# Kernel optimization log

Hardware: AMD Instinct MI355X
Metric: run time of the kernel (lower is better)

Reference implementation:

```python
import jax, jax.numpy as jnp
import numpy as np

B, N, D, H = 4, 1024, 1024, 16
DH = D // H  # 64
FF = 4 * D   # 4096


def _layernorm(x, w, b, eps=1e-5):
    mu = jnp.mean(x, axis=-1, keepdims=True)
    var = jnp.var(x, axis=-1, keepdims=True)
    return (x - mu) * jax.lax.rsqrt(var + eps) * w + b


def setup_inputs() -> dict:
    key = jax.random.key(0)
    ks = jax.random.split(key, 8)
    s = 0.02
    return {
        "x": jax.random.normal(ks[0], (B, N, D), jnp.float32),
        "ln1_w": jnp.ones((D,), jnp.float32),
        "ln1_b": jnp.zeros((D,), jnp.float32),
        "qkv_w": jax.random.normal(ks[1], (3 * D, D), jnp.float32) * s,
        "qkv_b": jnp.zeros((3 * D,), jnp.float32),
        "proj_l_w": jax.random.normal(ks[2], (H, H), jnp.float32) * s,
        "proj_l_b": jnp.zeros((H,), jnp.float32),
        "proj_w_w": jax.random.normal(ks[3], (H, H), jnp.float32) * s,
        "proj_w_b": jnp.zeros((H,), jnp.float32),
        "out_w": jax.random.normal(ks[4], (D, D), jnp.float32) * s,
        "out_b": jnp.zeros((D,), jnp.float32),
        "gamma1": jnp.ones((D,), jnp.float32),
        "ln2_w": jnp.ones((D,), jnp.float32),
        "ln2_b": jnp.zeros((D,), jnp.float32),
        "fc1_w": jax.random.normal(ks[5], (FF, D), jnp.float32) * s,
        "fc1_b": jnp.zeros((FF,), jnp.float32),
        "fc2_w": jax.random.normal(ks[6], (D, FF), jnp.float32) * s,
        "fc2_b": jnp.zeros((D,), jnp.float32),
        "gamma2": jnp.ones((D,), jnp.float32),
    }


def reference(x, ln1_w, ln1_b, qkv_w, qkv_b, proj_l_w, proj_l_b, proj_w_w,
              proj_w_b, out_w, out_b, gamma1, ln2_w, ln2_b, fc1_w, fc1_b,
              fc2_w, fc2_b, gamma2):
    # ---- LayerScale(TalkingHeadAttention) branch ----
    h = _layernorm(x, ln1_w, ln1_b)
    qkv = h @ qkv_w.T + qkv_b                      # [B,N,3D]
    q, k, v = jnp.split(qkv, 3, axis=-1)
    # [B,N,D] -> [B,H,N,DH]
    reshape = lambda t: t.reshape(B, N, H, DH).transpose(0, 2, 1, 3)
    q, k, v = reshape(q), reshape(k), reshape(v)
    attn = jnp.einsum("bhid,bhjd->bhij", q, k) * (DH ** -0.5)
    # talking-heads mixing before softmax (Linear over head dim)
    attn = jnp.einsum("bhij,gh->bgij", attn, proj_l_w) + proj_l_b[None, :, None, None]
    attn = jax.nn.softmax(attn, axis=-1)
    # talking-heads mixing after softmax
    attn = jnp.einsum("bhij,gh->bgij", attn, proj_w_w) + proj_w_b[None, :, None, None]
    o = jnp.einsum("bhij,bhjd->bhid", attn, v)     # [B,H,N,DH]
    o = o.transpose(0, 2, 1, 3).reshape(B, N, D)
    o = o @ out_w.T + out_b
    x = x + gamma1 * o
    # ---- LayerScale(MLP) branch ----
    h = _layernorm(x, ln2_w, ln2_b)
    h = jax.nn.gelu(h @ fc1_w.T + fc1_b)
    h = h @ fc2_w.T + fc2_b
    return x + gamma2 * h
```

## Files before the change

### kernel.cpp

```cpp
#include <hip/hip_runtime.h>


typedef _Float16 f16x8 __attribute__((ext_vector_type(8)));
typedef _Float16 f16x4 __attribute__((ext_vector_type(4)));
typedef _Float16 f16x2 __attribute__((ext_vector_type(2)));
typedef float f32x4 __attribute__((ext_vector_type(4)));

#define B_ 4
#define N_ 1024
#define D_ 1024
#define H_ 16
#define DH_ 64
#define FF_ 4096
#define M_ (B_ * N_)

__device__ __forceinline__ float gelu_act(float x) {
  float z = 0.7978845608028654f * (x + 0.044715f * x * x * x);
  return x / (1.0f + __expf(-2.0f * z));
}

__device__ __forceinline__ void ld_lds16(const _Float16* g, _Float16* l) {
  __builtin_amdgcn_global_load_lds((const __attribute__((address_space(1))) void*)g,
                                   (__attribute__((address_space(3))) void*)l, 16, 0, 0);
}

__device__ __forceinline__ int swz8(int i) {
  return (((i >> 2) << 1) ^ (i & 3)) & 7;
}
__device__ __forceinline__ int lds_off(int p, int i, int j) {
  int ch = ((j >> 3) ^ swz8(i) ^ ((p >> 2) << 1)) & 7;
  return p * 1032 + i * 64 + (ch << 3) + (j & 7);
}

__global__ __launch_bounds__(256) void cast_f32_f16(const float* __restrict__ in,
                                                    _Float16* __restrict__ out, int n) {
  int i = (blockIdx.x * 256 + threadIdx.x) * 4;
  if (i >= n) return;
  float4 v = *(const float4*)(in + i);
  f16x4 o;
  o[0] = (_Float16)v.x; o[1] = (_Float16)v.y; o[2] = (_Float16)v.z; o[3] = (_Float16)v.w;
  *(f16x4*)(out + i) = o;
}

__global__ __launch_bounds__(256) void prep_w(const float* __restrict__ W1,
                                              const float* __restrict__ W2,
                                              _Float16* __restrict__ w1f,
                                              _Float16* __restrict__ w2f) {
  int t = threadIdx.x;
  w1f[t] = (_Float16)W1[t];
  w2f[t] = (_Float16)W2[t];
}

__global__ __launch_bounds__(256) void vsum_k(const _Float16* __restrict__ vt,
                                              const float* __restrict__ b2,
                                              float* __restrict__ bsum) {
  int g = blockIdx.x, b = blockIdx.y;
  int t = threadIdx.x;
  int d = t >> 2, seg = t & 3;
  const _Float16* row = vt + (size_t)((b * H_ + g) * DH_ + d) * N_ + seg * 256;
  float s = 0.f;
  #pragma unroll
  for (int k = 0; k < 32; k++) {
    f16x8 v = *(const f16x8*)(row + k * 8);
    #pragma unroll
    for (int e = 0; e < 8; e++) s += (float)v[e];
  }
  s += __shfl_xor(s, 1);
  s += __shfl_xor(s, 2);
  if (seg == 0) bsum[b * D_ + g * 64 + d] = b2[g] * s;
}

__global__ __launch_bounds__(256) void ln_f16(const float* __restrict__ x,
                                              const float* __restrict__ w,
                                              const float* __restrict__ b,
                                              _Float16* __restrict__ out) {
  int row = blockIdx.x;
  int tid = threadIdx.x;
  const float* xr = x + (size_t)row * D_;
  float4 v = *(const float4*)(xr + tid * 4);
  float s = v.x + v.y + v.z + v.w;
  float sq = v.x * v.x + v.y * v.y + v.z * v.z + v.w * v.w;
  #pragma unroll
  for (int off = 32; off > 0; off >>= 1) {
    s += __shfl_down(s, off);
    sq += __shfl_down(sq, off);
  }
  __shared__ float red[8];
  int wave = tid >> 6, lane = tid & 63;
  if (lane == 0) { red[wave] = s; red[4 + wave] = sq; }
  __syncthreads();
  float ts = red[0] + red[1] + red[2] + red[3];
  float tq = red[4] + red[5] + red[6] + red[7];
  float mean = ts * (1.0f / (float)D_);
  float var = tq * (1.0f / (float)D_) - mean * mean;
  float rs = rsqrtf(var + 1e-5f);
  float4 wv = *(const float4*)(w + tid * 4);
  float4 bv = *(const float4*)(b + tid * 4);
  f16x4 o;
  o[0] = (_Float16)((v.x - mean) * rs * wv.x + bv.x);
  o[1] = (_Float16)((v.y - mean) * rs * wv.y + bv.y);
  o[2] = (_Float16)((v.z - mean) * rs * wv.z + bv.z);
  o[3] = (_Float16)((v.w - mean) * rs * wv.w + bv.w);
  *(f16x4*)(out + (size_t)row * D_ + tid * 4) = o;
}

template <int EPI, int BN>
__global__ __launch_bounds__(256, 3) void gemm_nt(
    const _Float16* __restrict__ A, const _Float16* __restrict__ W,
    const float* __restrict__ bias, int M, int N, int K,
    _Float16* __restrict__ outB, float* __restrict__ outF,
    const float* __restrict__ res, const float* __restrict__ gamma) {
  __shared__ _Float16 As[128 * 64];
  __shared__ _Float16 Bs[BN * 64];
  int tid = threadIdx.x;
  int wave = tid >> 6, lane = tid & 63;
  int quad = lane >> 4, l16 = lane & 15;
  int wm = wave >> 1, wn = wave & 1;
  int m0 = blockIdx.y * 128, n0 = blockIdx.x * BN;
  int lrow = lane >> 3, lcol = (lane & 7) * 8;
  const int NI = (BN == 128) ? 4 : 2;
  const int WN = (BN == 128) ? 64 : 32;

  f32x4 zero = {0.f, 0.f, 0.f, 0.f};
  f32x4 acc[4][NI];
  #pragma unroll
  for (int i = 0; i < 4; i++)
    #pragma unroll
    for (int j = 0; j < NI; j++) acc[i][j] = zero;

  for (int k0 = 0; k0 < K; k0 += 64) {
    __syncthreads();
    #pragma unroll
    for (int c = 0; c < 4; c++) {
      int rb = c * 32 + wave * 8;
      ld_lds16(A + (size_t)(m0 + rb + lrow) * K + k0 + lcol, As + rb * 64);
      if (BN == 128 || c < 2)
        ld_lds16(W + (size_t)(n0 + rb + lrow) * K + k0 + lcol, Bs + rb * 64);
    }
    __syncthreads();
    #pragma unroll
    for (int ks = 0; ks < 2; ks++) {
      int kk = ks * 32 + quad * 8;
      f16x8 a[4], bfr[NI];
      #pragma unroll
      for (int i = 0; i < 4; i++) a[i] = *(const f16x8*)(As + (wm * 64 + i * 16 + l16) * 64 + kk);
      #pragma unroll
      for (int i = 0; i < NI; i++) bfr[i] = *(const f16x8*)(Bs + (wn * WN + i * 16 + l16) * 64 + kk);
      #pragma unroll
      for (int mi = 0; mi < 4; mi++)
        #pragma unroll
        for (int ni = 0; ni < NI; ni++)
          acc[mi][ni] = __builtin_amdgcn_mfma_f32_16x16x32_f16(a[mi], bfr[ni], acc[mi][ni], 0, 0, 0);
    }
  }

  #pragma unroll
  for (int mi = 0; mi < 4; mi++) {
    int grow_base = m0 + wm * 64 + mi * 16 + quad * 4;
    #pragma unroll
    for (int ni = 0; ni < NI; ni++) {
      int gcol = n0 + wn * WN + ni * 16 + l16;
      float bb = bias[gcol];
      float gm = (EPI == 1) ? gamma[gcol] : 0.f;
      #pragma unroll
      for (int r = 0; r < 4; r++) {
        size_t oi = (size_t)(grow_base + r) * N + gcol;
        float c = acc[mi][ni][r] + bb;
        if (EPI == 0) {
          outB[oi] = (_Float16)c;
        } else if (EPI == 1) {
          outF[oi] = res[oi] + gm * c;
        } else {
          outB[oi] = (_Float16)gelu_act(c);
        }
      }
    }
  }
}

__global__ __launch_bounds__(256) void transpose_v(const _Float16* __restrict__ qkv,
                                                   _Float16* __restrict__ vt) {
  int jt = blockIdx.x;
  int h = blockIdx.y;
  int b = blockIdx.z;
  __shared__ _Float16 tl[64][68];
  int tid = threadIdx.x;
  int j0 = jt * 64;
  #pragma unroll
  for (int k = 0; k < 16; k++) {
    int idx = k * 256 + tid;
    int jr = idx >> 6, dc = idx & 63;
    tl[jr][dc] = qkv[(size_t)(b * N_ + j0 + jr) * (3 * D_) + 2 * D_ + h * 64 + dc];
  }
  __syncthreads();
  #pragma unroll
  for (int k = 0; k < 16; k++) {
    int idx = k * 256 + tid;
    int dr = idx >> 6, jc = idx & 63;
    vt[(size_t)((b * H_ + h) * DH_ + dr) * N_ + j0 + jc] = tl[jc][dr];
  }
}

__global__ __launch_bounds__(1024, 4) void attn_th(
    const _Float16* __restrict__ qkv, const _Float16* __restrict__ vt,
    const _Float16* __restrict__ w1f, const _Float16* __restrict__ w2f,
    const float* __restrict__ b1f, const float* __restrict__ bsum,
    _Float16* __restrict__ ob) {
  __shared__ __align__(16) _Float16 SP[2 * 16512];
  __shared__ float lsum[272];
  _Float16* Sp = SP;
  _Float16* Pp = SP + 16512;

  const int tid = threadIdx.x;
  const int wave = tid >> 6;
  const int lane = tid & 63;
  const int quad = lane >> 4, l16 = lane & 15;
  const int i0 = blockIdx.x * 16;
  const int b = blockIdx.y;
  const size_t bN = (size_t)b * N_;
  const f32x4 zero = {0.f, 0.f, 0.f, 0.f};

  f16x8 qf[2];
  #pragma unroll
  for (int ks = 0; ks < 2; ks++) {
    f16x8 q = *(const f16x8*)(qkv + (bN + i0 + l16) * 3072 + wave * 64 + ks * 32 + quad * 8);
    #pragma unroll
    for (int e = 0; e < 8; e++) q[e] = q[e] * (_Float16)0.125f;
    qf[ks] = q;
  }
  f16x4 w1a = *(const f16x4*)(w1f + l16 * 16 + quad * 4);
  float b1v = b1f[l16];
  f32x4 b1i = {b1v, b1v, b1v, b1v};

  f32x4 uacc[4];
  #pragma unroll
  for (int nt = 0; nt < 4; nt++) uacc[nt] = zero;
  float lacc = 0.f;

  for (int t = 0; t < 16; t++) {
    int j0 = t * 64;
    #pragma unroll
    for (int jb = 0; jb < 4; jb++) {
      const _Float16* kb = qkv + (bN + j0 + jb * 16 + l16) * 3072 + 1024 + wave * 64 + quad * 8;
      f32x4 s = __builtin_amdgcn_mfma_f32_16x16x32_f16(*(const f16x8*)kb, qf[0], zero, 0, 0, 0);
      s = __builtin_amdgcn_mfma_f32_16x16x32_f16(*(const f16x8*)(kb + 32), qf[1], s, 0, 0, 0);
      f16x4 sv;
      #pragma unroll
      for (int r = 0; r < 4; r++) sv[r] = (_Float16)s[r];
      *(f16x4*)(Sp + lds_off(wave, l16, jb * 16 + quad * 4)) = sv;
    }
    __syncthreads();
    #pragma unroll
    for (int cg = 0; cg < 4; cg++) {
      f16x4 sf;
      #pragma unroll
      for (int t4 = 0; t4 < 4; t4++)
        sf[t4] = Sp[lds_off(quad * 4 + t4, wave, cg * 16 + l16)];
      f32x4 a = __builtin_amdgcn_mfma_f32_16x16x16f16(sf, w1a, b1i, 0, 0, 0);
      f16x4 pv;
      #pragma unroll
      for (int r = 0; r < 4; r++) {
        float e = __expf(a[r]);
        lacc += e;
        pv[r] = (_Float16)e;
      }
      *(f16x4*)(Pp + lds_off(l16, wave, cg * 16 + quad * 4)) = pv;
    }
    __syncthreads();
    #pragma unroll
    for (int s = 0; s < 2; s++) {
      f16x8 pf = *(const f16x8*)(Pp + lds_off(wave, l16, s * 32 + quad * 8));
      #pragma unroll
      for (int nt = 0; nt < 4; nt++) {
        f16x8 vf = *(const f16x8*)(vt + (size_t)((b * H_ + wave) * DH_ + nt * 16 + l16) * N_ + j0 + s * 32 + quad * 8);
        uacc[nt] = __builtin_amdgcn_mfma_f32_16x16x32_f16(vf, pf, uacc[nt], 0, 0, 0);
      }
    }
  }

  lacc += __shfl_xor(lacc, 16);
  lacc += __shfl_xor(lacc, 32);
  __syncthreads();
  if (quad == 0) lsum[l16 * 17 + wave] = lacc;
  __syncthreads();
  float invl = 1.0f / lsum[wave * 17 + l16];

  _Float16* Uf = Sp;
  #pragma unroll
  for (int nt = 0; nt < 4; nt++) {
    f16x4 u;
    #pragma unroll
    for (int r = 0; r < 4; r++) u[r] = (_Float16)(uacc[nt][r] * invl);
    *(f16x4*)(Uf + wave * 1092 + l16 * 68 + nt * 16 + quad * 4) = u;
  }
  __syncthreads();

  f16x4 w2a = *(const f16x4*)(w2f + l16 * 16 + quad * 4);
  #pragma unroll
  for (int cg = 0; cg < 4; cg++) {
    f16x4 af;
    #pragma unroll
    for (int t4 = 0; t4 < 4; t4++)
      af[t4] = Uf[(quad * 4 + t4) * 1092 + wave * 68 + cg * 16 + l16];
    f32x4 o = __builtin_amdgcn_mfma_f32_16x16x16f16(af, w2a, zero, 0, 0, 0);
    f32x4 bs = *(const f32x4*)(bsum + b * D_ + l16 * 64 + cg * 16 + quad * 4);
    f16x4 ov;
    #pragma unroll
    for (int r = 0; r < 4; r++) ov[r] = (_Float16)(o[r] + bs[r]);
    *(f16x4*)(ob + (bN + i0 + wave) * D_ + l16 * 64 + cg * 16 + quad * 4) = ov;
  }
}

extern "C" void kernel_launch(void* const* d_in, const int* in_sizes, int n_in,
                              void* d_out, int out_size, void* d_ws, size_t ws_size,
                              hipStream_t stream) {
  const float* x      = (const float*)d_in[0];
  const float* ln1_w  = (const float*)d_in[1];
  const float* ln1_b  = (const float*)d_in[2];
  const float* qkv_w  = (const float*)d_in[3];
  const float* qkv_b  = (const float*)d_in[4];
  const float* plw    = (const float*)d_in[5];
  const float* plb    = (const float*)d_in[6];
  const float* pww    = (const float*)d_in[7];
  const float* pwb    = (const float*)d_in[8];
  const float* out_w  = (const float*)d_in[9];
  const float* out_b  = (const float*)d_in[10];
  const float* gamma1 = (const float*)d_in[11];
  const float* ln2_w  = (const float*)d_in[12];
  const float* ln2_b  = (const float*)d_in[13];
  const float* fc1_w  = (const float*)d_in[14];
  const float* fc1_b  = (const float*)d_in[15];
  const float* fc2_w  = (const float*)d_in[16];
  const float* fc2_b  = (const float*)d_in[17];
  const float* gamma2 = (const float*)d_in[18];
  float* out = (float*)d_out;

  char* ws = (char*)d_ws;
  _Float16* wq   = (_Float16*)(ws + 0);
  _Float16* wo   = (_Float16*)(ws + 6291456);
  _Float16* wf1  = (_Float16*)(ws + 8388608);
  _Float16* wf2  = (_Float16*)(ws + 16777216);
  float*    x1   = (float*)   (ws + 25165824);
  _Float16* ob   = (_Float16*)(ws + 41943040);
  _Float16* hb   = (_Float16*)(ws + 50331648);
  _Float16* qkvb = (_Float16*)(ws + 58720256);
  _Float16* vtb  = (_Float16*)(ws + 83886080);
  _Float16* fb   = (_Float16*)(ws + 58720256);
  _Float16* w1f  = (_Float16*)(ws + 8388608);
  _Float16* w2f  = (_Float16*)(ws + 8388608 + 512);
  float*    bsum = (float*)   (ws + 8388608 + 1024);
  if (ws_size < 92274688) return;

  cast_f32_f16<<<3072 * 1024 / 1024, 256, 0, stream>>>(qkv_w, wq, 3072 * 1024);
  cast_f32_f16<<<1024 * 1024 / 1024, 256, 0, stream>>>(out_w, wo, 1024 * 1024);
  prep_w<<<1, 256, 0, stream>>>(plw, pww, w1f, w2f);

  ln_f16<<<4096, 256, 0, stream>>>(x, ln1_w, ln1_b, hb);
  gemm_nt<0, 128><<<dim3(24, 32), 256, 0, stream>>>(hb, wq, qkv_b, M_, 3 * D_, D_, qkvb, nullptr, nullptr, nullptr);
  transpose_v<<<dim3(16, 16, 4), 256, 0, stream>>>(qkvb, vtb);
  vsum_k<<<dim3(16, 4), 256, 0, stream>>>(vtb, pwb, bsum);
  attn_th<<<dim3(64, 4), 1024, 0, stream>>>(qkvb, vtb, w1f, w2f, plb, bsum, ob);
  gemm_nt<1, 64><<<dim3(16, 32), 256, 0, stream>>>(ob, wo, out_b, M_, D_, D_, nullptr, x1, x, gamma1);

  cast_f32_f16<<<4096 * 1024 / 1024, 256, 0, stream>>>(fc1_w, wf1, 4096 * 1024);
  cast_f32_f16<<<4096 * 1024 / 1024, 256, 0, stream>>>(fc2_w, wf2, 4096 * 1024);

  ln_f16<<<4096, 256, 0, stream>>>(x1, ln2_w, ln2_b, hb);
  gemm_nt<2, 128><<<dim3(32, 32), 256, 0, stream>>>(hb, wf1, fc1_b, M_, FF_, D_, fb, nullptr, nullptr, nullptr);
  gemm_nt<1, 64><<<dim3(16, 32), 256, 0, stream>>>(fb, wf2, fc2_b, M_, D_, FF_, nullptr, out, x1, gamma2);
}
```

Measured before the change: 493.3 us.

## Prefetch K and V tiles into registers in attention loop; tune GEMM occupancy

The attention kernel now loads the next K tile into registers while the current tile is processed, and issues the V fragment loads before the barrier so their latency overlaps the softmax stage. The goal is to hide global memory latency in the QK and PV phases. Separately, the BN=64 GEMMs get a launch-bounds occupancy hint of 4 instead of 3. The extra live registers in the attention kernel could raise register pressure and lower occupancy, and the tighter occupancy bound on the GEMMs could force spills.

```diff
diff --git a/kernel.cpp b/kernel.cpp
--- a/kernel.cpp
+++ b/kernel.cpp
@@ -104,8 +104,8 @@
   *(f16x4*)(out + (size_t)row * D_ + tid * 4) = o;
 }
 
-template <int EPI, int BN>
-__global__ __launch_bounds__(256, 3) void gemm_nt(
+template <int EPI, int BN, int OCC>
+__global__ __launch_bounds__(256, OCC) void gemm_nt(
     const _Float16* __restrict__ A, const _Float16* __restrict__ W,
     const float* __restrict__ bias, int M, int N, int K,
     _Float16* __restrict__ outB, float* __restrict__ outF,
@@ -232,23 +232,45 @@
   float b1v = b1f[l16];
   f32x4 b1i = {b1v, b1v, b1v, b1v};
 
+  const _Float16* vbase = vt + (size_t)((b * H_ + wave) * DH_ + l16) * N_ + quad * 8;
+
   f32x4 uacc[4];
   #pragma unroll
   for (int nt = 0; nt < 4; nt++) uacc[nt] = zero;
   float lacc = 0.f;
 
+  f16x8 kcur[4][2];
+  auto loadK = [&](int j0) {
+    #pragma unroll
+    for (int jb = 0; jb < 4; jb++) {
+      const _Float16* kb = qkv + (bN + j0 + jb * 16 + l16) * 3072 + 1024 + wave * 64 + quad * 8;
+      kcur[jb][0] = *(const f16x8*)kb;
+      kcur[jb][1] = *(const f16x8*)(kb + 32);
+    }
+  };
+  loadK(0);
+
+  f16x8 vreg[4];
+
   for (int t = 0; t < 16; t++) {
     int j0 = t * 64;
+    f32x4 sres[4];
     #pragma unroll
     for (int jb = 0; jb < 4; jb++) {
-      const _Float16* kb = qkv + (bN + j0 + jb * 16 + l16) * 3072 + 1024 + wave * 64 + quad * 8;
-      f32x4 s = __builtin_amdgcn_mfma_f32_16x16x32_f16(*(const f16x8*)kb, qf[0], zero, 0, 0, 0);
-      s = __builtin_amdgcn_mfma_f32_16x16x32_f16(*(const f16x8*)(kb + 32), qf[1], s, 0, 0, 0);
+      f32x4 s = __builtin_amdgcn_mfma_f32_16x16x32_f16(kcur[jb][0], qf[0], zero, 0, 0, 0);
+      sres[jb] = __builtin_amdgcn_mfma_f32_16x16x32_f16(kcur[jb][1], qf[1], s, 0, 0, 0);
+    }
+    #pragma unroll
+    for (int jb = 0; jb < 4; jb++) {
       f16x4 sv;
       #pragma unroll
-      for (int r = 0; r < 4; r++) sv[r] = (_Float16)s[r];
+      for (int r = 0; r < 4; r++) sv[r] = (_Float16)sres[jb][r];
       *(f16x4*)(Sp + lds_off(wave, l16, jb * 16 + quad * 4)) = sv;
     }
+    if (t < 15) loadK(j0 + 64);
+    #pragma unroll
+    for (int nt = 0; nt < 4; nt++)
+      vreg[nt] = *(const f16x8*)(vbase + (size_t)(nt * 16) * N_ + j0);
     __syncthreads();
     #pragma unroll
     for (int cg = 0; cg < 4; cg++) {
@@ -267,14 +289,15 @@
       *(f16x4*)(Pp + lds_off(l16, wave, cg * 16 + quad * 4)) = pv;
     }
     __syncthreads();
-    #pragma unroll
-    for (int s = 0; s < 2; s++) {
-      f16x8 pf = *(const f16x8*)(Pp + lds_off(wave, l16, s * 32 + quad * 8));
-      #pragma unroll
-      for (int nt = 0; nt < 4; nt++) {
-        f16x8 vf = *(const f16x8*)(vt + (size_t)((b * H_ + wave) * DH_ + nt * 16 + l16) * N_ + j0 + s * 32 + quad * 8);
-        uacc[nt] = __builtin_amdgcn_mfma_f32_16x16x32_f16(vf, pf, uacc[nt], 0, 0, 0);
-      }
+    f16x8 pf0 = *(const f16x8*)(Pp + lds_off(wave, l16, quad * 8));
+    f16x8 pf1 = *(const f16x8*)(Pp + lds_off(wave, l16, 32 + quad * 8));
+    #pragma unroll
+    for (int nt = 0; nt < 4; nt++)
+      uacc[nt] = __builtin_amdgcn_mfma_f32_16x16x32_f16(vreg[nt], pf0, uacc[nt], 0, 0, 0);
+    #pragma unroll
+    for (int nt = 0; nt < 4; nt++) {
+      f16x8 vf = *(const f16x8*)(vbase + (size_t)(nt * 16) * N_ + j0 + 32);
+      uacc[nt] = __builtin_amdgcn_mfma_f32_16x16x32_f16(vf, pf1, uacc[nt], 0, 0, 0);
     }
   }
 
@@ -356,16 +379,16 @@
   prep_w<<<1, 256, 0, stream>>>(plw, pww, w1f, w2f);
 
   ln_f16<<<4096, 256, 0, stream>>>(x, ln1_w, ln1_b, hb);
-  gemm_nt<0, 128><<<dim3(24, 32), 256, 0, stream>>>(hb, wq, qkv_b, M_, 3 * D_, D_, qkvb, nullptr, nullptr, nullptr);
+  gemm_nt<0, 128, 3><<<dim3(24, 32), 256, 0, stream>>>(hb, wq, qkv_b, M_, 3 * D_, D_, qkvb, nullptr, nullptr, nullptr);
   transpose_v<<<dim3(16, 16, 4), 256, 0, stream>>>(qkvb, vtb);
   vsum_k<<<dim3(16, 4), 256, 0, stream>>>(vtb, pwb, bsum);
   attn_th<<<dim3(64, 4), 1024, 0, stream>>>(qkvb, vtb, w1f, w2f, plb, bsum, ob);
-  gemm_nt<1, 64><<<dim3(16, 32), 256, 0, stream>>>(ob, wo, out_b, M_, D_, D_, nullptr, x1, x, gamma1);
+  gemm_nt<1, 64, 4><<<dim3(16, 32), 256, 0, stream>>>(ob, wo, out_b, M_, D_, D_, nullptr, x1, x, gamma1);
 
   cast_f32_f16<<<4096 * 1024 / 1024, 256, 0, stream>>>(fc1_w, wf1, 4096 * 1024);
   cast_f32_f16<<<4096 * 1024 / 1024, 256, 0, stream>>>(fc2_w, wf2, 4096 * 1024);
 
   ln_f16<<<4096, 256, 0, stream>>>(x1, ln2_w, ln2_b, hb);
-  gemm_nt<2, 128><<<dim3(32, 32), 256, 0, stream>>>(hb, wf1, fc1_b, M_, FF_, D_, fb, nullptr, nullptr, nullptr);
-  gemm_nt<1, 64><<<dim3(16, 32), 256, 0, stream>>>(fb, wf2, fc2_b, M_, D_, FF_, nullptr, out, x1, gamma2);
-}
+  gemm_nt<2, 128, 3><<<dim3(32, 32), 256, 0, stream>>>(hb, wf1, fc1_b, M_, FF_, D_, fb, nullptr, nullptr, nullptr);
+  gemm_nt<1, 64, 4><<<dim3(16, 32), 256, 0, stream>>>(fb, wf2, fc2_b, M_, D_, FF_, nullptr, out, x1, gamma2);
+}
```

Measured after the change: 479.4 us. -2.8%, faster.
